# Performance work log

Measured on AMD Instinct MI355X. Metric: run time of the kernel, lower is better.

## Reference

```python
import jax, jax.numpy as jnp
import numpy as np

PATCH = 9  # local correlation window (must match init_kwargs)
B, C, H, W = 16, 512, 64, 64


def setup_inputs() -> dict:
    key = jax.random.key(0)
    k1, k2 = jax.random.split(key)
    feature1 = jax.random.normal(k1, (B, C, H, W), dtype=jnp.float32)
    feature2 = jax.random.normal(k2, (B, C, H, W), dtype=jnp.float32)
    return {"feature1": feature1, "feature2": feature2}


def _l2normalize(x):
    # matches torch: x / sqrt(sum(x^2, dim=1) + 1e-6)
    eps = 1e-6
    return x / jnp.sqrt(jnp.sum(x * x, axis=1, keepdims=True) + eps)


def reference(feature1, feature2):
    patch = PATCH
    max_d = patch // 2
    f1 = _l2normalize(feature1)
    f2 = _l2normalize(feature2)
    b, c, h, w = f1.shape
    # The torch code computes a full (hw x hw) corr volume then extracts
    # windowed diagonals with zero padding at borders. Equivalent direct form:
    # out[b, dh*patch+dw, y*w+x] = relu(<f2[:, y+dh-max_d, x+dw-max_d], f1[:, y, x]>)
    # with out-of-range f2 positions contributing exactly 0 (zero padding).
    f2p = jnp.pad(f2, ((0, 0), (0, 0), (max_d, max_d), (max_d, max_d)))
    # fixed small loop over patch^2 displacements (81), vectorized over b,c,h,w
    slices = [
        jnp.einsum('bchw,bchw->bhw', f2p[:, :, dh:dh + h, dw:dw + w], f1)
        for dh in range(patch) for dw in range(patch)
    ]
    corr = jnp.stack(slices, axis=1)            # (b, patch*patch, h, w)
    corr = corr.reshape(b, patch * patch, h * w)
    return jax.nn.relu(corr)
```

## Files before the change

kernel.cpp:

```cpp
#include <hip/hip_runtime.h>
#include <hip/hip_bf16.h>
#include <stdint.h>
#include <math.h>

#define NB 16
#define NC 512
#define NH 64
#define NW 64
#define HW 4096
#define TILE 16
#define HALO 24
#define HXP 32
#define KC 32
#define NCH (NC / KC)
#define ROWB 80
#define A_BASE 0
#define B_BASE (256 * ROWB)
#define S_BASE (B_BASE + 768 * ROWB)
#define LDS_BYTES (S_BASE + 1024 * 4)

using f32x4  = __attribute__((ext_vector_type(4))) float;
using bf16x8 = __attribute__((ext_vector_type(8))) short;
using i32x4  = __attribute__((ext_vector_type(4))) int;

__device__ __forceinline__ unsigned bf16r(float x) {
  unsigned u = __float_as_uint(x);
  u += 0x7fffu + ((u >> 16) & 1u);
  return u >> 16;
}

__global__ __launch_bounds__(512, 2)
void corr_mfma(const float* __restrict__ f1, const float* __restrict__ f2,
               float* __restrict__ out)
{
  alignas(16) __shared__ unsigned char smem[LDS_BYTES];
  float* snorm = reinterpret_cast<float*>(smem + S_BASE);

  const int tid  = threadIdx.x;

  const int blk  = blockIdx.x;
  const int xcd  = blk & 7;
  const int slot = blk >> 3;
  const int b    = xcd * 2 + (slot >> 4);
  const int t4   = slot & 15;
  const int y0   = (t4 >> 2) * TILE;
  const int x0   = (t4 & 3) * TILE;

  const int lane = tid & 63;
  const int lr   = lane & 15;
  const int lk   = lane >> 4;
  const int wv   = tid >> 6;

  const float* gptr[2];
  uint32_t     lbase[2];
  int          nidx[2];
  bool         ok[2];

  #pragma unroll
  for (int si = 0; si < 2; ++si) {
    const int s = tid + si * 512;
    nidx[si] = s;
    if (s < 256) {
      const int ty = s >> 4, tx = s & 15;
      gptr[si]  = f1 + (size_t)b * NC * HW + (size_t)(y0 + ty) * NW + (x0 + tx);
      lbase[si] = A_BASE + (uint32_t)s * ROWB;
      ok[si]    = true;
    } else {
      const int h  = s - 256;
      const int hy = h >> 5, hx = h & 31;
      const int yy = y0 - 4 + hy, xx = x0 - 4 + hx;
      const bool v = (hx < HALO) && ((unsigned)yy < NH) && ((unsigned)xx < NW);
      const size_t off = v ? ((size_t)b * NC * HW + (size_t)yy * NW + xx) : (size_t)0;
      gptr[si]  = f2 + off;
      lbase[si] = B_BASE + (uint32_t)h * ROWB;
      ok[si]    = v;
    }
  }

  f32x4 acc[2][9][2];
  #pragma unroll
  for (int i = 0; i < 2; ++i)
    #pragma unroll
    for (int j = 0; j < 9; ++j)
      #pragma unroll
      for (int k = 0; k < 2; ++k) {
        f32x4 z = {0.f, 0.f, 0.f, 0.f};
        acc[i][j][k] = z;
      }

  float ss[2] = {0.f, 0.f};

  for (int kc = 0; kc < NCH; ++kc) {
    #pragma unroll
    for (int si = 0; si < 2; ++si) {
      const float* gp = gptr[si] + (size_t)kc * KC * HW;
      float v[KC];
      if (ok[si]) {
        #pragma unroll
        for (int k = 0; k < KC; ++k) v[k] = gp[(size_t)k * HW];
      } else {
        #pragma unroll
        for (int k = 0; k < KC; ++k) v[k] = 0.f;
      }
      float ps = 0.f;
      #pragma unroll
      for (int k = 0; k < KC; ++k) ps = fmaf(v[k], v[k], ps);
      ss[si] += ps;

      unsigned char* lp = smem + lbase[si];
      #pragma unroll
      for (int j = 0; j < 4; ++j) {
        i32x4 w;
        #pragma unroll
        for (int q = 0; q < 4; ++q) {
          const unsigned lo = bf16r(v[j * 8 + 2 * q]);
          const unsigned hi = bf16r(v[j * 8 + 2 * q + 1]);
          w[q] = (int)((hi << 16) | lo);
        }
        *reinterpret_cast<i32x4*>(lp + j * 16) = w;
      }
    }
    __syncthreads();

    #pragma unroll
    for (int tyi = 0; tyi < 2; ++tyi) {
      const int ty = 2 * wv + tyi;
      const bf16x8 afr = *reinterpret_cast<const bf16x8*>(
          smem + A_BASE + (uint32_t)(ty * 16 + lr) * ROWB + lk * 16);
      #pragma unroll
      for (int dh = 0; dh < 9; ++dh) {
        const int hy = ty + dh;
        #pragma unroll
        for (int hx0 = 0; hx0 < 2; ++hx0) {
          const bf16x8 bfr = *reinterpret_cast<const bf16x8*>(
              smem + B_BASE + (uint32_t)(hy * HXP + hx0 * 16 + lr) * ROWB + lk * 16);
          acc[tyi][dh][hx0] =
              __builtin_amdgcn_mfma_f32_16x16x32_bf16(afr, bfr, acc[tyi][dh][hx0], 0, 0, 0);
        }
      }
    }
    __syncthreads();
  }

  snorm[nidx[0]] = ss[0];
  snorm[nidx[1]] = ss[1];
  __syncthreads();
  #pragma unroll
  for (int i = 0; i < 2; ++i) {
    const int idx = tid + i * 512;
    snorm[idx] = 1.0f / sqrtf(snorm[idx] + 1e-6f);
  }
  __syncthreads();

  float* op = out + (size_t)b * 81 * HW;
  #pragma unroll
  for (int tyi = 0; tyi < 2; ++tyi) {
    const int ty = 2 * wv + tyi;
    #pragma unroll
    for (int dh = 0; dh < 9; ++dh) {
      const int hy = ty + dh;
      #pragma unroll
      for (int hx0 = 0; hx0 < 2; ++hx0) {
        const f32x4 a4 = acc[tyi][dh][hx0];
        const float i2 = snorm[256 + hy * HXP + hx0 * 16 + lr];
        #pragma unroll
        for (int r = 0; r < 4; ++r) {
          const int m  = lk * 4 + r;
          const int dw = hx0 * 16 + lr - m;
          if (dw >= 0 && dw < 9) {
            const float i1 = snorm[ty * 16 + m];
            float val = a4[r] * i1 * i2;
            val = fmaxf(val, 0.f);
            op[(size_t)(dh * 9 + dw) * HW + (size_t)(y0 + ty) * NW + (x0 + m)] = val;
          }
        }
      }
    }
  }
}

extern "C" void kernel_launch(void* const* d_in, const int* in_sizes, int n_in,
                              void* d_out, int out_size, void* d_ws, size_t ws_size,
                              hipStream_t stream) {
  (void)in_sizes; (void)n_in; (void)out_size; (void)d_ws; (void)ws_size;
  const float* f1 = (const float*)d_in[0];
  const float* f2 = (const float*)d_in[1];
  float* out = (float*)d_out;
  corr_mfma<<<dim3(256), dim3(512), 0, stream>>>(f1, f2, out);
}
```

Measured before the change: 309.5 us.

## Halve tile height to 8x16, double grid, overlap halo columns in MFMA

Shrinks each block's output tile from 16x16 to 8x16 pixels, so the grid grows from 256 to 512 blocks. Each thread now loads a single row and each wave owns one tile row. The halo shrinks to 24 columns with no padding, and the two B fragments per row overlap at offsets 0 and 8 rather than 0 and 16. Launch bounds request 4 blocks per CU. The aim is more parallelism, fewer registers and less LDS so more blocks can run at once, at the cost of a larger fraction of redundant halo loads per output.

```diff
diff --git a/kernel.cpp b/kernel.cpp
--- a/kernel.cpp
+++ b/kernel.cpp
@@ -8,16 +8,19 @@
 #define NH 64
 #define NW 64
 #define HW 4096
-#define TILE 16
-#define HALO 24
-#define HXP 32
+#define TILE_H 8
+#define TILE_W 16
+#define HALO_H 16
+#define HALO_W 24
+#define NHALO (HALO_H * HALO_W)
+#define A_ROWS (TILE_H * TILE_W)
 #define KC 32
 #define NCH (NC / KC)
 #define ROWB 80
 #define A_BASE 0
-#define B_BASE (256 * ROWB)
-#define S_BASE (B_BASE + 768 * ROWB)
-#define LDS_BYTES (S_BASE + 1024 * 4)
+#define B_BASE (A_ROWS * ROWB)
+#define S_BASE (B_BASE + NHALO * ROWB)
+#define LDS_BYTES (S_BASE + 512 * 4)
 
 using f32x4  = __attribute__((ext_vector_type(4))) float;
 using bf16x8 = __attribute__((ext_vector_type(8))) short;
@@ -29,73 +32,66 @@
   return u >> 16;
 }
 
-__global__ __launch_bounds__(512, 2)
+__global__ __launch_bounds__(512, 4)
 void corr_mfma(const float* __restrict__ f1, const float* __restrict__ f2,
                float* __restrict__ out)
 {
   alignas(16) __shared__ unsigned char smem[LDS_BYTES];
   float* snorm = reinterpret_cast<float*>(smem + S_BASE);
 
-  const int tid  = threadIdx.x;
+  const int tid = threadIdx.x;
 
   const int blk  = blockIdx.x;
   const int xcd  = blk & 7;
   const int slot = blk >> 3;
-  const int b    = xcd * 2 + (slot >> 4);
-  const int t4   = slot & 15;
-  const int y0   = (t4 >> 2) * TILE;
-  const int x0   = (t4 & 3) * TILE;
+  const int b    = xcd * 2 + (slot >> 5);
+  const int t5   = slot & 31;
+  const int y0   = (t5 >> 2) * TILE_H;
+  const int x0   = (t5 & 3) * TILE_W;
 
   const int lane = tid & 63;
   const int lr   = lane & 15;
   const int lk   = lane >> 4;
   const int wv   = tid >> 6;
 
-  const float* gptr[2];
-  uint32_t     lbase[2];
-  int          nidx[2];
-  bool         ok[2];
-
-  #pragma unroll
-  for (int si = 0; si < 2; ++si) {
-    const int s = tid + si * 512;
-    nidx[si] = s;
-    if (s < 256) {
+  const float* gptr;
+  uint32_t     lbase;
+  bool         ok;
+  {
+    const int s = tid;
+    if (s < A_ROWS) {
       const int ty = s >> 4, tx = s & 15;
-      gptr[si]  = f1 + (size_t)b * NC * HW + (size_t)(y0 + ty) * NW + (x0 + tx);
-      lbase[si] = A_BASE + (uint32_t)s * ROWB;
-      ok[si]    = true;
+      gptr  = f1 + (size_t)b * NC * HW + (size_t)(y0 + ty) * NW + (x0 + tx);
+      lbase = A_BASE + (uint32_t)s * ROWB;
+      ok    = true;
     } else {
-      const int h  = s - 256;
-      const int hy = h >> 5, hx = h & 31;
+      const int h  = s - A_ROWS;
+      const int hy = h / HALO_W, hx = h % HALO_W;
       const int yy = y0 - 4 + hy, xx = x0 - 4 + hx;
-      const bool v = (hx < HALO) && ((unsigned)yy < NH) && ((unsigned)xx < NW);
+      const bool v = ((unsigned)yy < NH) && ((unsigned)xx < NW);
       const size_t off = v ? ((size_t)b * NC * HW + (size_t)yy * NW + xx) : (size_t)0;
-      gptr[si]  = f2 + off;
-      lbase[si] = B_BASE + (uint32_t)h * ROWB;
-      ok[si]    = v;
+      gptr  = f2 + off;
+      lbase = B_BASE + (uint32_t)h * ROWB;
+      ok    = v;
     }
   }
 
-  f32x4 acc[2][9][2];
+  f32x4 acc[9][2];
   #pragma unroll
-  for (int i = 0; i < 2; ++i)
+  for (int j = 0; j < 9; ++j)
     #pragma unroll
-    for (int j = 0; j < 9; ++j)
-      #pragma unroll
-      for (int k = 0; k < 2; ++k) {
-        f32x4 z = {0.f, 0.f, 0.f, 0.f};
-        acc[i][j][k] = z;
-      }
+    for (int k = 0; k < 2; ++k) {
+      f32x4 z = {0.f, 0.f, 0.f, 0.f};
+      acc[j][k] = z;
+    }
 
-  float ss[2] = {0.f, 0.f};
+  float ss = 0.f;
 
   for (int kc = 0; kc < NCH; ++kc) {
-    #pragma unroll
-    for (int si = 0; si < 2; ++si) {
-      const float* gp = gptr[si] + (size_t)kc * KC * HW;
+    {
+      const float* gp = gptr + (size_t)kc * KC * HW;
       float v[KC];
-      if (ok[si]) {
+      if (ok) {
         #pragma unroll
         for (int k = 0; k < KC; ++k) v[k] = gp[(size_t)k * HW];
       } else {
@@ -105,9 +101,9 @@
       float ps = 0.f;
       #pragma unroll
       for (int k = 0; k < KC; ++k) ps = fmaf(v[k], v[k], ps);
-      ss[si] += ps;
+      ss += ps;
 
-      unsigned char* lp = smem + lbase[si];
+      unsigned char* lp = smem + lbase;
       #pragma unroll
       for (int j = 0; j < 4; ++j) {
         i32x4 w;
@@ -122,57 +118,47 @@
     }
     __syncthreads();
 
+    const bf16x8 afr = *reinterpret_cast<const bf16x8*>(
+        smem + A_BASE + (uint32_t)(wv * 16 + lr) * ROWB + lk * 16);
     #pragma unroll
-    for (int tyi = 0; tyi < 2; ++tyi) {
-      const int ty = 2 * wv + tyi;
-      const bf16x8 afr = *reinterpret_cast<const bf16x8*>(
-          smem + A_BASE + (uint32_t)(ty * 16 + lr) * ROWB + lk * 16);
+    for (int dh = 0; dh < 9; ++dh) {
+      const int hy = wv + dh;
       #pragma unroll
-      for (int dh = 0; dh < 9; ++dh) {
-        const int hy = ty + dh;
-        #pragma unroll
-        for (int hx0 = 0; hx0 < 2; ++hx0) {
-          const bf16x8 bfr = *reinterpret_cast<const bf16x8*>(
-              smem + B_BASE + (uint32_t)(hy * HXP + hx0 * 16 + lr) * ROWB + lk * 16);
-          acc[tyi][dh][hx0] =
-              __builtin_amdgcn_mfma_f32_16x16x32_bf16(afr, bfr, acc[tyi][dh][hx0], 0, 0, 0);
-        }
+      for (int hx0 = 0; hx0 < 2; ++hx0) {
+        const bf16x8 bfr = *reinterpret_cast<const bf16x8*>(
+            smem + B_BASE + (uint32_t)(hy * HALO_W + hx0 * 8 + lr) * ROWB + lk * 16);
+        acc[dh][hx0] =
+            __builtin_amdgcn_mfma_f32_16x16x32_bf16(afr, bfr, acc[dh][hx0], 0, 0, 0);
       }
     }
     __syncthreads();
   }
 
-  snorm[nidx[0]] = ss[0];
-  snorm[nidx[1]] = ss[1];
+  snorm[tid] = ss;
   __syncthreads();
-  #pragma unroll
-  for (int i = 0; i < 2; ++i) {
-    const int idx = tid + i * 512;
-    snorm[idx] = 1.0f / sqrtf(snorm[idx] + 1e-6f);
+  {
+    const float t = snorm[tid];
+    snorm[tid] = 1.0f / sqrtf(t + 1e-6f);
   }
   __syncthreads();
 
   float* op = out + (size_t)b * 81 * HW;
   #pragma unroll
-  for (int tyi = 0; tyi < 2; ++tyi) {
-    const int ty = 2 * wv + tyi;
+  for (int dh = 0; dh < 9; ++dh) {
+    const int hy = wv + dh;
     #pragma unroll
-    for (int dh = 0; dh < 9; ++dh) {
-      const int hy = ty + dh;
+    for (int hx0 = 0; hx0 < 2; ++hx0) {
+      const f32x4 a4 = acc[dh][hx0];
+      const float i2 = snorm[A_ROWS + hy * HALO_W + hx0 * 8 + lr];
       #pragma unroll
-      for (int hx0 = 0; hx0 < 2; ++hx0) {
-        const f32x4 a4 = acc[tyi][dh][hx0];
-        const float i2 = snorm[256 + hy * HXP + hx0 * 16 + lr];
-        #pragma unroll
-        for (int r = 0; r < 4; ++r) {
-          const int m  = lk * 4 + r;
-          const int dw = hx0 * 16 + lr - m;
-          if (dw >= 0 && dw < 9) {
-            const float i1 = snorm[ty * 16 + m];
-            float val = a4[r] * i1 * i2;
-            val = fmaxf(val, 0.f);
-            op[(size_t)(dh * 9 + dw) * HW + (size_t)(y0 + ty) * NW + (x0 + m)] = val;
-          }
+      for (int r = 0; r < 4; ++r) {
+        const int m  = lk * 4 + r;
+        const int dw = hx0 * 8 + lr - m;
+        if (dw >= 0 && dw < 9) {
+          const float i1 = snorm[wv * 16 + m];
+          float val = a4[r] * i1 * i2;
+          val = fmaxf(val, 0.f);
+          op[(size_t)(dh * 9 + dw) * HW + (size_t)(y0 + wv) * NW + (x0 + m)] = val;
         }
       }
     }
@@ -186,5 +172,5 @@
   const float* f1 = (const float*)d_in[0];
   const float* f2 = (const float*)d_in[1];
   float* out = (float*)d_out;
-  corr_mfma<<<dim3(256), dim3(512), 0, stream>>>(f1, f2, out);
+  corr_mfma<<<dim3(512), dim3(512), 0, stream>>>(f1, f2, out);
 }
```

New measurement: 316.1 us. 2.1% more time.
